# Kernel tuning notes

Measured on AMD Instinct MI355X. Metric: run time of the kernel, lower is better.

Reference implementation:

```python
import jax, jax.numpy as jnp
import numpy as np
from jax import lax

N, C = 32768, 128
K5, K3 = 125, 27
EPS = 1e-5


def sparse_conv(feats, nbr, W):
    """Gather-GEMM-accumulate sparse conv.
    feats: [N, Cin]; nbr: [K, N] int (neighbor row per kernel tap); W: [K, Cin, Cout].
    out[i] = sum_k feats[nbr[k, i]] @ W[k]
    """
    def step(acc, kw):
        idx, Wk = kw
        return acc + feats[idx] @ Wk, None
    acc0 = jnp.zeros((feats.shape[0], W.shape[-1]), feats.dtype)
    acc, _ = lax.scan(step, acc0, (nbr, W))
    return acc


def batchnorm(x, gamma, beta):
    mu = jnp.mean(x, axis=0)
    var = jnp.mean(jnp.square(x - mu), axis=0)
    return (x - mu) * lax.rsqrt(var + EPS) * gamma + beta


def setup_inputs() -> dict:
    key = jax.random.key(0)
    ks = jax.random.split(key, 12)
    s1 = 1.0 / np.sqrt(C)            # 1x1 conv fan-in
    s5 = 1.0 / np.sqrt(C * K5)       # 5^3 conv fan-in
    s3 = 1.0 / np.sqrt(C * K3)       # 3^3 conv fan-in
    return {
        "x": jax.random.normal(ks[0], (N, C), jnp.float32),
        "Wa1": jax.random.normal(ks[1], (C, C), jnp.float32) * s1,
        "Wv1": jax.random.normal(ks[2], (C, C), jnp.float32) * s1,
        "W5": jax.random.normal(ks[3], (K5, C, C), jnp.float32) * s5,
        "W31": jax.random.normal(ks[4], (K3, C, C), jnp.float32) * s3,
        "W32": jax.random.normal(ks[5], (K3, C, C), jnp.float32) * s3,
        "gamma1": jnp.ones((C,), jnp.float32),
        "beta1": jnp.zeros((C,), jnp.float32),
        "gamma2": jnp.ones((C,), jnp.float32),
        "beta2": jnp.zeros((C,), jnp.float32),
        "nbr5": jax.random.randint(ks[6], (N, K5), 0, N, jnp.int32),
        "nbr3a": jax.random.randint(ks[7], (N, K3), 0, N, jnp.int32),
        "nbr3b": jax.random.randint(ks[8], (N, K3), 0, N, jnp.int32),
    }


def reference(x, Wa1, Wv1, W5, W31, W32, gamma1, beta1, gamma2, beta2, nbr5, nbr3a, nbr3b):
    residual = x
    # a branch: 1x1 conv (stride=1 -> kernel_size 1) then 5^3 sparse conv
    a = x @ Wa1
    a = sparse_conv(a, nbr5.T, W5)
    # v branch: 1x1 conv
    v = x @ Wv1
    # gated elementwise mult
    out = a * v
    # conv1 -> BN1 -> (dropout=identity) + residual
    out = sparse_conv(out, nbr3a.T, W31)
    out = batchnorm(out, gamma1, beta1)
    out = out + residual
    residual = out
    out = jax.nn.relu(out)
    # conv2 -> BN2 -> (dropout=identity) + residual -> relu
    out = sparse_conv(out, nbr3b.T, W32)
    out = batchnorm(out, gamma2, beta2)
    out = out + residual
    out = jax.nn.relu(out)
    return out
```

## Files before the change

kernel.cpp:

```cpp
#include <hip/hip_runtime.h>
#include <stdint.h>


#define NPTS 32768
#define C 128
#define EPS 1e-5f

typedef unsigned short u16;
using bfrag = __attribute__((ext_vector_type(8))) short;
using f32x4 = __attribute__((ext_vector_type(4))) float;

__device__ __forceinline__ float b2f(u16 u) {
  union { unsigned int i; float f; } x;
  x.i = ((unsigned int)u) << 16;
  return x.f;
}
__device__ __forceinline__ u16 f2b(float f) {
  union { float f; unsigned int i; } x;
  x.f = f;
  unsigned int r = x.i + 0x7FFFu + ((x.i >> 16) & 1u);
  return (u16)(r >> 16);
}

__device__ __forceinline__ void g2l16(const void* g, void* l) {
  __builtin_amdgcn_global_load_lds(
      (const __attribute__((address_space(1))) unsigned int*)g,
      (__attribute__((address_space(3))) unsigned int*)l,
      16, 0, 0);
}

#define GG_W(N)                                                            \
  asm volatile("s_waitcnt vmcnt(" #N ")" ::: "memory");                    \
  __builtin_amdgcn_sched_barrier(0)

#define GG_WB(N)                                                           \
  asm volatile("s_waitcnt vmcnt(" #N ") lgkmcnt(0)" ::: "memory");         \
  __builtin_amdgcn_s_barrier();                                            \
  __builtin_amdgcn_sched_barrier(0)

template <int NTAPS, int EPI>
__global__ __launch_bounds__(512, 1)
void gg_kernel(const u16* __restrict__ src, const u16* __restrict__ WT,
               const int* __restrict__ nbr, u16* __restrict__ outb,
               float* __restrict__ outf, const u16* __restrict__ vmul) {
  __shared__ uint4 lds[8192];
  char* const base = (char*)lds;
  char* const bufs[4] = {base, base + 32768, base + 65536, base + 98304};

  const int tid  = threadIdx.x;
  const int lane = tid & 63;
  const int wv   = tid >> 6;
  const int wr   = wv >> 1, wc = wv & 1;
  const int lsub = lane >> 4, lm = lane & 15;
  const int r8   = lane >> 3;
  const int cs8  = lane & 7;
  const int row0 = blockIdx.x * 128;

  f32x4 acc[2][4];
#pragma unroll
  for (int i = 0; i < 2; i++)
#pragma unroll
    for (int j = 0; j < 4; j++) acc[i][j] = (f32x4)(0.0f);

  auto loadIdx = [&](int (&d)[2], int st) {
    const int tp = st < NTAPS ? st : st - NTAPS;
#pragma unroll
    for (int j = 0; j < 2; j++) {
      const int gr = row0 + wv * 16 + j * 8 + r8;
      const int* p = nbr + (size_t)gr * NTAPS + tp;
      asm volatile("global_load_dword %0, %1, off"
                   : "=v"(d[j]) : "v"(p) : "memory");
    }
  };

  auto stageA = [&](char* buf, const int (&id)[2], int st) {
    const int h = st < NTAPS ? 0 : 1;
#pragma unroll
    for (int j = 0; j < 2; j++) {
      const char* gp = (const char*)src + ((size_t)(unsigned)id[j] << 8)
                     + (h << 7) + ((cs8 ^ r8) << 4);
      g2l16(gp, buf + (wv * 16 + j * 8) * 128);
    }
  };

  auto stageB = [&](char* buf, int st) {
    const int tp = st < NTAPS ? st : st - NTAPS;
    const int h = st < NTAPS ? 0 : 1;
    const char* wt = (const char*)WT + ((size_t)tp << 15) + (h << 7);
#pragma unroll
    for (int j = 0; j < 2; j++) {
      const int col = wv * 16 + j * 8 + r8;
      g2l16(wt + ((size_t)col << 8) + ((cs8 ^ r8) << 4),
            buf + 16384 + (wv * 16 + j * 8) * 128);
    }
  };

  auto computeS = [&](const char* buf) {
#pragma unroll
    for (int kk2 = 0; kk2 < 2; kk2++) {
      bfrag af[2], bg[4];
#pragma unroll
      for (int rt = 0; rt < 2; rt++) {
        const int row = wr * 32 + rt * 16 + lm;
        af[rt] = *(const bfrag*)(buf + row * 128
                                 + (((kk2 * 4 + lsub) ^ (row & 7)) << 4));
      }
#pragma unroll
      for (int ct = 0; ct < 4; ct++) {
        const int col = wc * 64 + ct * 16 + lm;
        bg[ct] = *(const bfrag*)(buf + 16384 + col * 128
                                 + (((kk2 * 4 + lsub) ^ (col & 7)) << 4));
      }
#pragma unroll
      for (int rt = 0; rt < 2; rt++)
#pragma unroll
        for (int ct = 0; ct < 4; ct++)
          acc[rt][ct] = __builtin_amdgcn_mfma_f32_16x16x32_bf16(
              af[rt], bg[ct], acc[rt][ct], 0, 0, 0);
    }
  };

  if constexpr (NTAPS == 1) {
    bfrag aR[2][2][2];
#pragma unroll
    for (int rt = 0; rt < 2; rt++) {
      const char* rb = (const char*)src
          + (size_t)(row0 + wr * 32 + rt * 16 + lm) * 256 + lsub * 16;
      aR[0][rt][0] = *(const bfrag*)(rb);
      aR[0][rt][1] = *(const bfrag*)(rb + 64);
      aR[1][rt][0] = *(const bfrag*)(rb + 128);
      aR[1][rt][1] = *(const bfrag*)(rb + 192);
    }
    stageB(bufs[0], 0);
    stageB(bufs[1], 1);
    GG_WB(0);
#pragma unroll
    for (int h = 0; h < 2; h++) {
      const char* buf = bufs[h];
#pragma unroll
      for (int kk2 = 0; kk2 < 2; kk2++) {
        bfrag bg[4];
#pragma unroll
        for (int ct = 0; ct < 4; ct++) {
          const int col = wc * 64 + ct * 16 + lm;
          bg[ct] = *(const bfrag*)(buf + 16384 + col * 128
                                   + (((kk2 * 4 + lsub) ^ (col & 7)) << 4));
        }
#pragma unroll
        for (int rt = 0; rt < 2; rt++)
#pragma unroll
          for (int ct = 0; ct < 4; ct++)
            acc[rt][ct] = __builtin_amdgcn_mfma_f32_16x16x32_bf16(
                aR[h][rt][kk2], bg[ct], acc[rt][ct], 0, 0, 0);
      }
    }
  } else {
    constexpr int S = 2 * NTAPS;
    int idr[4][2], ip0[2], ip1[2], ip2[2];
    loadIdx(ip0, 0); loadIdx(ip1, 1); loadIdx(ip2, 2);
    GG_W(0);
    stageA(bufs[0], ip0, 0); stageB(bufs[0], 0); loadIdx(idr[1], 3);
    stageA(bufs[1], ip1, 1); stageB(bufs[1], 1); loadIdx(idr[2], 4);
    stageA(bufs[2], ip2, 2); stageB(bufs[2], 2); loadIdx(idr[3], 5);

#define GG_SUB(p)                                                          \
    GG_WB(12);                                                             \
    stageA(bufs[((p) + 3) & 3], idr[((p) + 1) & 3], s + (p) + 3);          \
    stageB(bufs[((p) + 3) & 3], s + (p) + 3);                              \
    loadIdx(idr[(p) & 3], s + (p) + 6);                                    \
    computeS(bufs[(p) & 3]);

#pragma unroll 1
    for (int s = 0; s < S - 6; s += 4) {
      GG_SUB(0)
      GG_SUB(1)
      GG_SUB(2)
      GG_SUB(3)
    }
#undef GG_SUB

    GG_WB(12);
    stageA(bufs[3], idr[1], S - 3); stageB(bufs[3], S - 3);
    computeS(bufs[0]);
    GG_WB(10);
    stageA(bufs[0], idr[2], S - 2); stageB(bufs[0], S - 2);
    computeS(bufs[1]);
    GG_WB(8);
    stageA(bufs[1], idr[3], S - 1); stageB(bufs[1], S - 1);
    computeS(bufs[2]);
    GG_WB(8);
    computeS(bufs[3]);
    GG_WB(4);
    computeS(bufs[0]);
    GG_WB(0);
    computeS(bufs[1]);
  }

#pragma unroll
  for (int rt = 0; rt < 2; rt++) {
    const int rowb = row0 + wr * 32 + rt * 16 + lsub * 4;
#pragma unroll
    for (int ct = 0; ct < 4; ct++) {
      const int c = wc * 64 + ct * 16 + lm;
#pragma unroll
      for (int reg = 0; reg < 4; reg++) {
        const size_t off = (size_t)(rowb + reg) * C + c;
        const float v = acc[rt][ct][reg];
        if (EPI == 0)      outb[off] = f2b(v);
        else if (EPI == 1) outb[off] = f2b(v * b2f(vmul[off]));
        else               outf[off] = v;
      }
    }
  }
}

__global__ __launch_bounds__(256)
void cvt_kernel(const float* __restrict__ x, u16* __restrict__ xb) {
  const int i = (blockIdx.x * 256 + threadIdx.x) * 4;
  const float4 v = *(const float4*)(x + i);
  ushort4 o;
  o.x = f2b(v.x); o.y = f2b(v.y); o.z = f2b(v.z); o.w = f2b(v.w);
  *(ushort4*)(xb + i) = o;
}

__global__ __launch_bounds__(256)
void wt_kernel(const float* __restrict__ W5, const float* __restrict__ W31,
               const float* __restrict__ W32, const float* __restrict__ Wa1,
               const float* __restrict__ Wv1,
               u16* __restrict__ T5, u16* __restrict__ T31, u16* __restrict__ T32,
               u16* __restrict__ Ta1, u16* __restrict__ Tv1) {
  const int b = blockIdx.x;
  const float* w;
  u16* o;
  if (b < 125)       { w = W5  + (size_t)b * 16384;         o = T5  + (size_t)b * 16384; }
  else if (b < 152)  { w = W31 + (size_t)(b - 125) * 16384; o = T31 + (size_t)(b - 125) * 16384; }
  else if (b < 179)  { w = W32 + (size_t)(b - 152) * 16384; o = T32 + (size_t)(b - 152) * 16384; }
  else if (b == 179) { w = Wa1; o = Ta1; }
  else               { w = Wv1; o = Tv1; }
  __shared__ u16 tile[128 * 129];
  for (int i = threadIdx.x; i < C * C; i += 256)
    tile[(i & 127) * 129 + (i >> 7)] = f2b(w[i]);
  __syncthreads();
  for (int i = threadIdx.x; i < C * C; i += 256)
    o[i] = tile[(i >> 7) * 129 + (i & 127)];
}

__global__ __launch_bounds__(256)
void bnp_kernel(const float* __restrict__ t, float* __restrict__ psum,
                float* __restrict__ psq) {
  const int b = blockIdx.x;
  const int c = threadIdx.x & 127;
  const int h = threadIdx.x >> 7;
  const float* p = t + (size_t)(b * 128 + h * 64) * C + c;
  float s = 0.f, q = 0.f;
#pragma unroll 8
  for (int j = 0; j < 64; j++) {
    const float v = p[(size_t)j * C];
    s += v; q += v * v;
  }
  __shared__ float ls[256], lq[256];
  ls[threadIdx.x] = s; lq[threadIdx.x] = q;
  __syncthreads();
  if (h == 0) {
    psum[b * 128 + c] = ls[c] + ls[c + 128];
    psq[b * 128 + c]  = lq[c] + lq[c + 128];
  }
}

__global__ __launch_bounds__(256)
void bnfin_kernel(const float* __restrict__ psum, const float* __restrict__ psq,
                  const float* __restrict__ gamma, const float* __restrict__ beta,
                  float* __restrict__ scale, float* __restrict__ shift) {
  const int c = blockIdx.x;
  const int t = threadIdx.x;
  float s = psum[(size_t)t * 128 + c];
  float q = psq[(size_t)t * 128 + c];
#pragma unroll
  for (int o = 32; o > 0; o >>= 1) {
    s += __shfl_down(s, o);
    q += __shfl_down(q, o);
  }
  __shared__ float ls[4], lq[4];
  if ((t & 63) == 0) { ls[t >> 6] = s; lq[t >> 6] = q; }
  __syncthreads();
  if (t == 0) {
    s = ls[0] + ls[1] + ls[2] + ls[3];
    q = lq[0] + lq[1] + lq[2] + lq[3];
    const float mean = s * (1.0f / NPTS);
    const float var  = q * (1.0f / NPTS) - mean * mean;
    const float sc   = rsqrtf(var + EPS) * gamma[c];
    scale[c] = sc;
    shift[c] = beta[c] - mean * sc;
  }
}

__global__ __launch_bounds__(256)
void ew1_kernel(const float* __restrict__ t, const float* __restrict__ x,
                const float* __restrict__ scale, const float* __restrict__ shift,
                u16* __restrict__ res, u16* __restrict__ h) {
  const int i = blockIdx.x * 256 + threadIdx.x;
  const int c = i & 127;
  const float o = t[i] * scale[c] + shift[c] + x[i];
  res[i] = f2b(o);
  h[i] = f2b(o < 0.f ? 0.f : o);
}

__global__ __launch_bounds__(256)
void ew2_kernel(const float* __restrict__ t2, const u16* __restrict__ res,
                const float* __restrict__ scale, const float* __restrict__ shift,
                float* __restrict__ y) {
  const int i = blockIdx.x * 256 + threadIdx.x;
  const int c = i & 127;
  const float o = t2[i] * scale[c] + shift[c] + b2f(res[i]);
  y[i] = o < 0.f ? 0.f : o;
}

extern "C" void kernel_launch(void* const* d_in, const int* in_sizes, int n_in,
                              void* d_out, int out_size, void* d_ws, size_t ws_size,
                              hipStream_t stream) {
  (void)in_sizes; (void)n_in; (void)out_size; (void)ws_size;

  const float* x   = (const float*)d_in[0];
  const float* Wa1 = (const float*)d_in[1];
  const float* Wv1 = (const float*)d_in[2];
  const float* W5  = (const float*)d_in[3];
  const float* W31 = (const float*)d_in[4];
  const float* W32 = (const float*)d_in[5];
  const float* g1  = (const float*)d_in[6];
  const float* b1  = (const float*)d_in[7];
  const float* g2  = (const float*)d_in[8];
  const float* b2  = (const float*)d_in[9];
  const int* nbr5  = (const int*)d_in[10];
  const int* nbr3a = (const int*)d_in[11];
  const int* nbr3b = (const int*)d_in[12];

  char* w = (char*)d_ws;
  u16* WT5  = (u16*)w; w += 4096000;
  u16* WT31 = (u16*)w; w += 884736;
  u16* WT32 = (u16*)w; w += 884736;
  u16* WTa1 = (u16*)w; w += 32768;
  u16* WTv1 = (u16*)w; w += 32768;
  char* AV  = w;       w += 16777216;
  u16*   a_b = (u16*)AV;
  u16*   v_b = (u16*)(AV + 8388608);
  float* tf  = (float*)AV;
  u16* g_b  = (u16*)w; w += 8388608;
  u16* h_b  = (u16*)w; w += 8388608;
  u16* xb   = h_b;
  float* psum = (float*)w; w += 131072;
  float* psq  = (float*)w; w += 131072;
  float* sc1  = (float*)w; w += 512;
  float* sh1  = (float*)w; w += 512;
  float* sc2  = (float*)w; w += 512;
  float* sh2  = (float*)w; w += 512;

  const dim3 B512(512), GG(NPTS / 128), B256(256), GBN(256), GEW(NPTS * C / 256);
  float* yout = (float*)d_out;

  cvt_kernel<<<dim3(NPTS * C / 1024), B256, 0, stream>>>(x, xb);
  wt_kernel<<<dim3(181), B256, 0, stream>>>(W5, W31, W32, Wa1, Wv1,
                                            WT5, WT31, WT32, WTa1, WTv1);

  gg_kernel<1, 0><<<GG, B512, 0, stream>>>(xb, WTa1, nullptr, a_b, nullptr, nullptr);
  gg_kernel<1, 0><<<GG, B512, 0, stream>>>(xb, WTv1, nullptr, v_b, nullptr, nullptr);

  gg_kernel<125, 1><<<GG, B512, 0, stream>>>(a_b, WT5, nbr5, g_b, nullptr, v_b);

  gg_kernel<27, 2><<<GG, B512, 0, stream>>>(g_b, WT31, nbr3a, nullptr, tf, nullptr);
  bnp_kernel<<<GBN, B256, 0, stream>>>(tf, psum, psq);
  bnfin_kernel<<<dim3(128), B256, 0, stream>>>(psum, psq, g1, b1, sc1, sh1);
  ew1_kernel<<<GEW, B256, 0, stream>>>(tf, x, sc1, sh1, g_b, h_b);

  gg_kernel<27, 2><<<GG, B512, 0, stream>>>(h_b, WT32, nbr3b, nullptr, tf, nullptr);
  bnp_kernel<<<GBN, B256, 0, stream>>>(tf, psum, psq);
  bnfin_kernel<<<dim3(128), B256, 0, stream>>>(psum, psq, g2, b2, sc2, sh2);
  ew2_kernel<<<GEW, B256, 0, stream>>>(tf, g_b, sc2, sh2, yout);
}
```

Before: 376.9 us.

## Split K across wave groups with larger per-wave tiles and LDS reduction

Waves are now split into two groups, each handling half of the K slice of every staged tile. Each wave computes a 64x64 output tile instead of 32x64, which raises MFMA work per fragment load and cuts LDS reads per MFMA. The two partial accumulators are summed through LDS in the epilogue, and the 1x1 path now stages A through LDS like the gather path. This doubles accumulator registers and adds an LDS reduction and barriers at the end, while only half the waves do the global stores.

Result: no change. 376.0 us (-0.2%).

```diff
diff --git a/kernel.cpp b/kernel.cpp
--- a/kernel.cpp
+++ b/kernel.cpp
@@ -50,15 +50,17 @@
   const int tid  = threadIdx.x;
   const int lane = tid & 63;
   const int wv   = tid >> 6;
-  const int wr   = wv >> 1, wc = wv & 1;
+  const int wq   = wv & 3;
+  const int wr   = wq >> 1, wc = wq & 1;
+  const int kk2w = wv >> 2;
   const int lsub = lane >> 4, lm = lane & 15;
   const int r8   = lane >> 3;
   const int cs8  = lane & 7;
   const int row0 = blockIdx.x * 128;
 
-  f32x4 acc[2][4];
-#pragma unroll
-  for (int i = 0; i < 2; i++)
+  f32x4 acc[4][4];
+#pragma unroll
+  for (int i = 0; i < 4; i++)
 #pragma unroll
     for (int j = 0; j < 4; j++) acc[i][j] = (f32x4)(0.0f);
 
@@ -96,64 +98,36 @@
   };
 
   auto computeS = [&](const char* buf) {
-#pragma unroll
-    for (int kk2 = 0; kk2 < 2; kk2++) {
-      bfrag af[2], bg[4];
-#pragma unroll
-      for (int rt = 0; rt < 2; rt++) {
-        const int row = wr * 32 + rt * 16 + lm;
-        af[rt] = *(const bfrag*)(buf + row * 128
-                                 + (((kk2 * 4 + lsub) ^ (row & 7)) << 4));
-      }
-#pragma unroll
-      for (int ct = 0; ct < 4; ct++) {
-        const int col = wc * 64 + ct * 16 + lm;
-        bg[ct] = *(const bfrag*)(buf + 16384 + col * 128
-                                 + (((kk2 * 4 + lsub) ^ (col & 7)) << 4));
-      }
-#pragma unroll
-      for (int rt = 0; rt < 2; rt++)
-#pragma unroll
-        for (int ct = 0; ct < 4; ct++)
-          acc[rt][ct] = __builtin_amdgcn_mfma_f32_16x16x32_bf16(
-              af[rt], bg[ct], acc[rt][ct], 0, 0, 0);
-    }
+    bfrag af[4], bg[4];
+#pragma unroll
+    for (int rt = 0; rt < 4; rt++) {
+      const int row = wr * 64 + rt * 16 + lm;
+      af[rt] = *(const bfrag*)(buf + row * 128
+                               + (((kk2w * 4 + lsub) ^ (row & 7)) << 4));
+    }
+#pragma unroll
+    for (int ct = 0; ct < 4; ct++) {
+      const int col = wc * 64 + ct * 16 + lm;
+      bg[ct] = *(const bfrag*)(buf + 16384 + col * 128
+                               + (((kk2w * 4 + lsub) ^ (col & 7)) << 4));
+    }
+#pragma unroll
+    for (int rt = 0; rt < 4; rt++)
+#pragma unroll
+      for (int ct = 0; ct < 4; ct++)
+        acc[rt][ct] = __builtin_amdgcn_mfma_f32_16x16x32_bf16(
+            af[rt], bg[ct], acc[rt][ct], 0, 0, 0);
   };
 
   if constexpr (NTAPS == 1) {
-    bfrag aR[2][2][2];
-#pragma unroll
-    for (int rt = 0; rt < 2; rt++) {
-      const char* rb = (const char*)src
-          + (size_t)(row0 + wr * 32 + rt * 16 + lm) * 256 + lsub * 16;
-      aR[0][rt][0] = *(const bfrag*)(rb);
-      aR[0][rt][1] = *(const bfrag*)(rb + 64);
-      aR[1][rt][0] = *(const bfrag*)(rb + 128);
-      aR[1][rt][1] = *(const bfrag*)(rb + 192);
-    }
-    stageB(bufs[0], 0);
-    stageB(bufs[1], 1);
+    int idv[2];
+#pragma unroll
+    for (int j = 0; j < 2; j++) idv[j] = row0 + wv * 16 + j * 8 + r8;
+    stageA(bufs[0], idv, 0); stageB(bufs[0], 0);
+    stageA(bufs[1], idv, 1); stageB(bufs[1], 1);
     GG_WB(0);
-#pragma unroll
-    for (int h = 0; h < 2; h++) {
-      const char* buf = bufs[h];
-#pragma unroll
-      for (int kk2 = 0; kk2 < 2; kk2++) {
-        bfrag bg[4];
-#pragma unroll
-        for (int ct = 0; ct < 4; ct++) {
-          const int col = wc * 64 + ct * 16 + lm;
-          bg[ct] = *(const bfrag*)(buf + 16384 + col * 128
-                                   + (((kk2 * 4 + lsub) ^ (col & 7)) << 4));
-        }
-#pragma unroll
-        for (int rt = 0; rt < 2; rt++)
-#pragma unroll
-          for (int ct = 0; ct < 4; ct++)
-            acc[rt][ct] = __builtin_amdgcn_mfma_f32_16x16x32_bf16(
-                aR[h][rt][kk2], bg[ct], acc[rt][ct], 0, 0, 0);
-      }
-    }
+    computeS(bufs[0]);
+    computeS(bufs[1]);
   } else {
     constexpr int S = 2 * NTAPS;
     int idr[4][2], ip0[2], ip1[2], ip2[2];
@@ -196,19 +170,39 @@
     computeS(bufs[1]);
   }
 
-#pragma unroll
-  for (int rt = 0; rt < 2; rt++) {
-    const int rowb = row0 + wr * 32 + rt * 16 + lsub * 4;
-#pragma unroll
-    for (int ct = 0; ct < 4; ct++) {
-      const int c = wc * 64 + ct * 16 + lm;
-#pragma unroll
-      for (int reg = 0; reg < 4; reg++) {
-        const size_t off = (size_t)(rowb + reg) * C + c;
-        const float v = acc[rt][ct][reg];
-        if (EPI == 0)      outb[off] = f2b(v);
-        else if (EPI == 1) outb[off] = f2b(v * b2f(vmul[off]));
-        else               outf[off] = v;
+  asm volatile("s_waitcnt lgkmcnt(0)" ::: "memory");
+  __builtin_amdgcn_s_barrier();
+  __builtin_amdgcn_sched_barrier(0);
+  if (wv >= 4) {
+    char* dst = base + (size_t)(wv - 4) * 16384 + lane * 16;
+#pragma unroll
+    for (int rt = 0; rt < 4; rt++)
+#pragma unroll
+      for (int ct = 0; ct < 4; ct++)
+        *(f32x4*)(dst + (rt * 4 + ct) * 1024) = acc[rt][ct];
+  }
+  asm volatile("s_waitcnt lgkmcnt(0)" ::: "memory");
+  __builtin_amdgcn_s_barrier();
+  __builtin_amdgcn_sched_barrier(0);
+
+  if (wv < 4) {
+    const char* psrc = base + (size_t)wv * 16384 + lane * 16;
+#pragma unroll
+    for (int rt = 0; rt < 4; rt++) {
+      const int rowb = row0 + wr * 64 + rt * 16 + lsub * 4;
+#pragma unroll
+      for (int ct = 0; ct < 4; ct++) {
+        const f32x4 part = *(const f32x4*)(psrc + (rt * 4 + ct) * 1024);
+        const f32x4 v4 = acc[rt][ct] + part;
+        const int c = wc * 64 + ct * 16 + lm;
+#pragma unroll
+        for (int reg = 0; reg < 4; reg++) {
+          const size_t off = (size_t)(rowb + reg) * C + c;
+          const float v = v4[reg];
+          if (EPI == 0)      outb[off] = f2b(v);
+          else if (EPI == 1) outb[off] = f2b(v * b2f(vmul[off]));
+          else               outf[off] = v;
+        }
       }
     }
   }
```
